# Kernel tuning notes

Measured on AMD Instinct MI355X. Metric: run time of the kernel, lower is better.

Reference implementation:

```python
import jax, jax.numpy as jnp
import numpy as np

SLOPE = 10.0  # sigmoid sharpness in custom_activation


def setup_inputs() -> dict:
    key = jax.random.key(0)
    kA, kB = jax.random.split(key)
    N, L, F = 64, 512, 2048  # batch, maxLengthSize, lenForbidden
    A = jax.random.normal(kA, (N, L, 2), dtype=jnp.float32)
    B = jax.random.normal(kB, (1, 2, F), dtype=jnp.float32)
    return {"A": A, "B": B}


def reference(A, B):
    # C = A.unsqueeze(3) - B.unsqueeze(0): (N, L, 2, 1) - (1, 1, 2, F) -> (N, L, 2, F)
    C = A[..., None] - B[None, ...]
    g = jax.nn.sigmoid(SLOPE * C) * jax.nn.sigmoid(-SLOPE * C)
    # split channels (dim 2, size 2) and take elementwise minimum -> (N, L, F)
    m = jnp.minimum(g[:, :, 0, :], g[:, :, 1, :])
    # MaxPool2d((1, lenForbidden), stride=1) over width F == max over forbidden axis -> (N, L)
    pooled = jnp.max(m, axis=-1)
    # squeeze then min over dim 1 with keepdim -> (N, 1)
    return jnp.min(pooled, axis=1, keepdims=True)
```

## Files before the change

kernel.cpp:

```cpp
#include <hip/hip_runtime.h>
#include <hip/hip_bf16.h>


#define NN 64
#define LL 512
#define FF 2048
#define P  8

__global__ __launch_bounds__(256) void psl_reduce_kernel(
    const float* __restrict__ A, const float* __restrict__ B,
    float* __restrict__ ws) {
  const int wave = __builtin_amdgcn_readfirstlane(threadIdx.x >> 6);
  const int lane = threadIdx.x & 63;
  const int p_base = blockIdx.x * 32 + wave * P;

  float ax[P], ay[P];
#pragma unroll
  for (int i = 0; i < P; ++i) {
    const float2 a = ((const float2*)A)[p_base + i];
    ax[i] = a.x; ay[i] = a.y;
  }

  const float4* __restrict__ B0 = (const float4*)B;
  const float4* __restrict__ B1 = (const float4*)(B + FF);

  float m[P];
#pragma unroll
  for (int i = 0; i < P; ++i) m[i] = 3.4e38f;

#pragma unroll
  for (int it = 0; it < FF / 256; ++it) {
    const int idx = it * 64 + lane;
    const float4 b0 = B0[idx];
    const float4 b1 = B1[idx];
#pragma unroll
    for (int i = 0; i < P; ++i) {
      const float v0 = fmaxf(fabsf(ax[i] - b0.x), fabsf(ay[i] - b1.x));
      const float v1 = fmaxf(fabsf(ax[i] - b0.y), fabsf(ay[i] - b1.y));
      const float v2 = fmaxf(fabsf(ax[i] - b0.z), fabsf(ay[i] - b1.z));
      const float v3 = fmaxf(fabsf(ax[i] - b0.w), fabsf(ay[i] - b1.w));
      m[i] = fminf(m[i], fminf(fminf(fminf(v0, v1), v2), v3));
    }
  }

  float t = 0.0f;
#pragma unroll
  for (int i = 0; i < P; ++i) {
#pragma unroll
    for (int off = 32; off; off >>= 1)
      m[i] = fminf(m[i], __shfl_xor(m[i], off));
    t = fmaxf(t, m[i]);
  }

  __shared__ float sm[4];
  if (lane == 0) sm[wave] = t;
  __syncthreads();
  if (threadIdx.x == 0)
    ws[blockIdx.x] = fmaxf(fmaxf(sm[0], sm[1]), fmaxf(sm[2], sm[3]));
}

__global__ __launch_bounds__(64) void psl_finalize_kernel(
    const float* __restrict__ ws, float* __restrict__ out) {
  const int n = threadIdx.x;
  float t = 0.0f;
#pragma unroll
  for (int j = 0; j < (LL / 32); ++j)
    t = fmaxf(t, ws[n * (LL / 32) + j]);
  out[n] = (1.0f / (1.0f + expf(-10.0f * t))) *
           (1.0f / (1.0f + expf( 10.0f * t)));
}

extern "C" void kernel_launch(void* const* d_in, const int* in_sizes, int n_in,
                              void* d_out, int out_size, void* d_ws, size_t ws_size,
                              hipStream_t stream) {
  const float* A = (const float*)d_in[0];
  const float* B = (const float*)d_in[1];
  float* out     = (float*)d_out;
  float* ws      = (float*)d_ws;

  const int blocks = (NN * LL) / 32;
  psl_reduce_kernel<<<blocks, 256, 0, stream>>>(A, B, ws);
  psl_finalize_kernel<<<1, 64, 0, stream>>>(ws, out);
}
```

Measured before the change: 63.30 us.

## Fuse reduce and finalize kernels via cooperative grid sync

Merges the two-kernel reduction into a single cooperative kernel that publishes per-block maxima with release stores, synchronizes the whole grid, then has block 0 compute the final per-batch result. This aims to remove the second kernel launch and its inter-kernel gap. It requires all 1024 blocks to be co-resident for the cooperative launch, and grid sync adds its own barrier cost across every block.

```diff
diff --git a/kernel.cpp b/kernel.cpp
--- a/kernel.cpp
+++ b/kernel.cpp
@@ -1,5 +1,7 @@
 #include <hip/hip_runtime.h>
-#include <hip/hip_bf16.h>
+#include <hip/hip_cooperative_groups.h>
+
+namespace cg = cooperative_groups;
 
 
 #define NN 64
@@ -7,9 +9,9 @@
 #define FF 2048
 #define P  8
 
-__global__ __launch_bounds__(256) void psl_reduce_kernel(
+__global__ __launch_bounds__(256) void psl_fused_kernel(
     const float* __restrict__ A, const float* __restrict__ B,
-    float* __restrict__ ws) {
+    float* __restrict__ ws, float* __restrict__ out) {
   const int wave = __builtin_amdgcn_readfirstlane(threadIdx.x >> 6);
   const int lane = threadIdx.x & 63;
   const int p_base = blockIdx.x * 32 + wave * P;
@@ -55,19 +57,25 @@
   __shared__ float sm[4];
   if (lane == 0) sm[wave] = t;
   __syncthreads();
-  if (threadIdx.x == 0)
-    ws[blockIdx.x] = fmaxf(fmaxf(sm[0], sm[1]), fmaxf(sm[2], sm[3]));
-}
+  if (threadIdx.x == 0) {
+    const float bt = fmaxf(fmaxf(sm[0], sm[1]), fmaxf(sm[2], sm[3]));
+    __hip_atomic_store(&ws[blockIdx.x], bt, __ATOMIC_RELEASE,
+                       __HIP_MEMORY_SCOPE_AGENT);
+  }
 
-__global__ __launch_bounds__(64) void psl_finalize_kernel(
-    const float* __restrict__ ws, float* __restrict__ out) {
-  const int n = threadIdx.x;
-  float t = 0.0f;
+  cg::this_grid().sync();
+
+  if (blockIdx.x == 0 && threadIdx.x < NN) {
+    const int n = threadIdx.x;
+    float t2 = 0.0f;
 #pragma unroll
-  for (int j = 0; j < (LL / 32); ++j)
-    t = fmaxf(t, ws[n * (LL / 32) + j]);
-  out[n] = (1.0f / (1.0f + expf(-10.0f * t))) *
-           (1.0f / (1.0f + expf( 10.0f * t)));
+    for (int j = 0; j < (LL / 32); ++j)
+      t2 = fmaxf(t2, __hip_atomic_load(&ws[n * (LL / 32) + j],
+                                       __ATOMIC_ACQUIRE,
+                                       __HIP_MEMORY_SCOPE_AGENT));
+    out[n] = (1.0f / (1.0f + expf(-10.0f * t2))) *
+             (1.0f / (1.0f + expf( 10.0f * t2)));
+  }
 }
 
 extern "C" void kernel_launch(void* const* d_in, const int* in_sizes, int n_in,
@@ -78,7 +86,9 @@
   float* out     = (float*)d_out;
   float* ws      = (float*)d_ws;
 
-  const int blocks = (NN * LL) / 32;
-  psl_reduce_kernel<<<blocks, 256, 0, stream>>>(A, B, ws);
-  psl_finalize_kernel<<<1, 64, 0, stream>>>(ws, out);
+  void* args[] = {(void*)&A, (void*)&B, (void*)&ws, (void*)&out};
+  dim3 grid((NN * LL) / 32);
+  dim3 block(256);
+  hipLaunchCooperativeKernel((void*)psl_fused_kernel, grid, block, args, 0,
+                             stream);
 }
```

Result: slower. 206.1 us (+225.6%).
